# Performance work log

Hardware: AMD Instinct MI355X
Metric: run time of the kernel (lower is better)

Reference implementation:

```python
import jax, jax.numpy as jnp
import numpy as np

S, E, H, T = 8192, 100, 768, 7  # seq_len, embed_dim, per-dir hidden, tagset


def setup_inputs() -> dict:
    key = jax.random.key(0)
    ks = jax.random.split(key, 16)
    s = 0.05
    return {
        "sentence": jax.random.normal(ks[0], (S, 1, E), dtype=jnp.float32),
        # forward-direction LSTM params (PyTorch gate order i,f,g,o)
        "w_ih_f": jax.random.normal(ks[1], (4 * H, E), dtype=jnp.float32) * s,
        "w_hh_f": jax.random.normal(ks[2], (4 * H, H), dtype=jnp.float32) * s,
        "b_ih_f": jnp.zeros((4 * H,), jnp.float32),
        "b_hh_f": jnp.zeros((4 * H,), jnp.float32),
        # backward-direction LSTM params
        "w_ih_b": jax.random.normal(ks[3], (4 * H, E), dtype=jnp.float32) * s,
        "w_hh_b": jax.random.normal(ks[4], (4 * H, H), dtype=jnp.float32) * s,
        "b_ih_b": jnp.zeros((4 * H,), jnp.float32),
        "b_hh_b": jnp.zeros((4 * H,), jnp.float32),
        # random initial states, as in init_hidden() (shape (2,1,H): dir, batch, H)
        "h0": jax.random.normal(ks[5], (2, 1, H), dtype=jnp.float32),
        "c0": jax.random.normal(ks[6], (2, 1, H), dtype=jnp.float32),
        # hidden2tag linear
        "w_tag": jax.random.normal(ks[7], (T, 2 * H), dtype=jnp.float32) * s,
        "b_tag": jnp.zeros((T,), jnp.float32),
        # CRF params
        "transitions": jax.random.normal(ks[8], (T, T), dtype=jnp.float32) * 0.1,
        "start_trans": jax.random.normal(ks[9], (T,), dtype=jnp.float32) * 0.1,
        "end_trans": jax.random.normal(ks[10], (T,), dtype=jnp.float32) * 0.1,
    }


def _lstm_dir(x, w_ih, w_hh, b_ih, b_hh, h0, c0):
    """Single-direction LSTM. x: (S,E); returns hidden states (S,H)."""
    xp = x @ w_ih.T + b_ih  # (S, 4H) input projection, one big GEMM

    def step(carry, xt):
        h, c = carry
        g = xt + h @ w_hh.T + b_hh
        i, f, gg, o = jnp.split(g, 4)
        i = jax.nn.sigmoid(i)
        f = jax.nn.sigmoid(f)
        gg = jnp.tanh(gg)
        o = jax.nn.sigmoid(o)
        c = f * c + i * gg
        h = o * jnp.tanh(c)
        return (h, c), h

    _, hs = jax.lax.scan(step, (h0, c0), xp)
    return hs


def reference(sentence, w_ih_f, w_hh_f, b_ih_f, b_hh_f,
              w_ih_b, w_hh_b, b_ih_b, b_hh_b, h0, c0,
              w_tag, b_tag, transitions, start_trans, end_trans):
    x = sentence[:, 0, :]  # (S, E), batch of 1
    hf = _lstm_dir(x, w_ih_f, w_hh_f, b_ih_f, b_hh_f, h0[0, 0], c0[0, 0])
    hb = _lstm_dir(x[::-1], w_ih_b, w_hh_b, b_ih_b, b_hh_b, h0[1, 0], c0[1, 0])[::-1]
    lstm_out = jnp.concatenate([hf, hb], axis=-1)  # (S, 2H)
    feats = lstm_out @ w_tag.T + b_tag             # (S, T) emission scores

    # CRF forward algorithm (log-partition) -- sequential DP over tiny tagset
    alpha0 = start_trans + feats[0]

    def crf_step(alpha, emit):
        alpha = jax.nn.logsumexp(alpha[:, None] + transitions + emit[None, :], axis=0)
        return alpha, None

    alpha, _ = jax.lax.scan(crf_step, alpha0, feats[1:])
    return jax.nn.logsumexp(alpha + end_trans)  # scalar log Z
```

## Files before the change

kernel.cpp:

```cpp
#include <hip/hip_runtime.h>
#include <stdint.h>

#define S_LEN 8192
#define E_DIM 100
#define H_DIM 768
#define NTAG 7
#define G4 3072
#define NBLK 96
#define NCHUNK 128
#define POLL_LIMIT 150000

typedef unsigned short u16;
typedef unsigned long long u64;
typedef __attribute__((ext_vector_type(4))) float f4v;

__device__ int g_isbf16;

__device__ __forceinline__ u16 f2bf(float f) {
    union { float f; unsigned u; } v; v.f = f;
    unsigned b = v.u;
    unsigned r = (b + 0x7FFFu + ((b >> 16) & 1u)) >> 16;
    return (u16)r;
}
__device__ __forceinline__ float bf2f(u16 u) {
    union { unsigned u; float f; } v; v.u = ((unsigned)u) << 16;
    return v.f;
}
__device__ __forceinline__ float getv(const void* p, size_t i, int isbf) {
    return isbf ? bf2f(((const u16*)p)[i]) : ((const float*)p)[i];
}
__device__ __forceinline__ float sigm(float x) {
    return __builtin_amdgcn_rcpf(1.0f + __expf(-x));
}
__device__ __forceinline__ float ftanh(float x) {
    return 2.0f * __builtin_amdgcn_rcpf(1.0f + __expf(-2.0f * x)) - 1.0f;
}

__global__ void detect(const void* x) {
    __shared__ int cnt;
    if (threadIdx.x == 0) cnt = 0;
    __syncthreads();
    unsigned v = ((const u16*)x)[2 * threadIdx.x];
    int e = (v >> 7) & 0xFF;
    if (e >= 110 && e <= 132) atomicAdd(&cnt, 1);
    __syncthreads();
    if (threadIdx.x == 0) g_isbf16 = (cnt >= 100) ? 1 : 0;
}

__global__ void prep(const void* bihf, const void* bhhf,
                     const void* bihb, const void* bhhb,
                     const void* h0, const void* c0,
                     float* __restrict__ cst, float* __restrict__ bias,
                     u64* __restrict__ slots) {
    const int isbf = g_isbf16;
    int i = blockIdx.x * blockDim.x + threadIdx.x;
    if (i < G4) {
        bias[i]      = getv(bihf, i, isbf) + getv(bhhf, i, isbf);
        bias[G4 + i] = getv(bihb, i, isbf) + getv(bhhb, i, isbf);
    }
    if (i < 2 * H_DIM) cst[i] = getv(c0, i, isbf);
    if (i < 384) {
        unsigned pf = (unsigned)f2bf(getv(h0, 2 * i, isbf))
                    | ((unsigned)f2bf(getv(h0, 2 * i + 1, isbf)) << 16);
        unsigned pb = (unsigned)f2bf(getv(h0, H_DIM + 2 * i, isbf))
                    | ((unsigned)f2bf(getv(h0, H_DIM + 2 * i + 1, isbf)) << 16);
        slots[i]        = (u64)pf;
        slots[768 + i]  = (u64)pb;
        slots[384 + i]  = 0xFFFFFFFF00000000ull;
        slots[1152 + i] = 0xFFFFFFFF00000000ull;
    }
}

#define PISSUE(A, B)                                                     \
    asm volatile("global_load_dwordx2 %0, %2, off sc0 sc1\n\t"           \
                 "global_load_dwordx2 %1, %3, off sc0 sc1"               \
                 : "=&v"(A), "=&v"(B) : "v"(pa), "v"(pb) : "memory")
#define PWAIT2(A, B)                                                     \
    asm volatile("s_waitcnt vmcnt(2)" : "+v"(A), "+v"(B))
#define PDRAIN4(A, B, C, D)                                              \
    asm volatile("s_waitcnt vmcnt(0)"                                    \
                 : "+v"(A), "+v"(B), "+v"(C), "+v"(D))

__global__ __launch_bounds__(256, 1) void lstm_persist(
        const void* x,
        const void* wihf, const void* whhf,
        const void* wihb, const void* whhb,
        u16* __restrict__ hfseq, u16* __restrict__ hbseq,
        float* __restrict__ cstate, const float* __restrict__ biasv,
        u64* __restrict__ slots, int* __restrict__ bail) {
    const int isbf = g_isbf16;
    const int bid = blockIdx.x;
    const int dir = (bid >= NBLK) ? 1 : 0;
    const int blk = bid - dir * NBLK;
    const int tid = threadIdx.x;
    const int wave = tid >> 6, lane = tid & 63;
    const int seg = tid & 7;
    const int row = tid >> 3;
    const int gamma = row & 3;
    const int uloc = row >> 2;
    const int u = blk * 8 + uloc;
    const size_t grow = (size_t)(gamma * H_DIM + u);
    u16* hseq = dir ? hbseq : hfseq;
    u64* myslots = slots + (size_t)dir * 768;
    const void* Wih = dir ? wihb : wihf;
    const void* Whh = dir ? whhb : whhf;

    __shared__ float sh[1600];

    float whh[96], wih[13];
    if (isbf) {
        const unsigned* p = (const unsigned*)((const u16*)Whh + grow * H_DIM + seg * 96);
        #pragma unroll
        for (int i = 0; i < 48; ++i) {
            unsigned q = p[i];
            whh[2 * i] = bf2f((u16)q); whh[2 * i + 1] = bf2f((u16)(q >> 16));
        }
        const unsigned* px = (const unsigned*)((const u16*)Wih + grow * E_DIM + seg * 12);
        #pragma unroll
        for (int i = 0; i < 6; ++i) {
            unsigned q = px[i];
            wih[2 * i] = bf2f((u16)q); wih[2 * i + 1] = bf2f((u16)(q >> 16));
        }
        wih[12] = (seg < 4) ? bf2f(((const u16*)Wih)[grow * E_DIM + 96 + seg]) : 0.f;
    } else {
        const float* p = (const float*)Whh + grow * H_DIM + seg * 96;
        #pragma unroll
        for (int i = 0; i < 96; ++i) whh[i] = p[i];
        const float* px = (const float*)Wih + grow * E_DIM + seg * 12;
        #pragma unroll
        for (int i = 0; i < 12; ++i) wih[i] = px[i];
        wih[12] = (seg < 4) ? ((const float*)Wih)[grow * E_DIM + 96 + seg] : 0.f;
    }
    const float bias_r = biasv[dir * G4 + grow];
    const int uhalf = blk * 8 + wave * 2 + (lane >> 5);
    float cst = cstate[dir * H_DIM + uhalf];

    const int sA = wave * 96 + lane;
    const int sB = (lane < 32) ? (wave * 96 + 64 + lane) : sA;
    const int oA = (2 * wave + (lane >= 48)) * 100 + 2 * lane - ((lane >= 48) ? 96 : 0);
    const int oB = (2 * wave + 1) * 100 + 32 + 2 * lane;
    const int pubslot = blk * 4 + wave;

    float    xf[13];
    unsigned xu[6];
    u16      xt16 = 0;
    auto load_x = [&](int t) {
        const int sx = dir ? (S_LEN - 1 - t) : t;
        if (isbf) {
            const unsigned* xr = (const unsigned*)((const u16*)x + (size_t)sx * E_DIM + seg * 12);
            #pragma unroll
            for (int i = 0; i < 6; ++i) xu[i] = xr[i];
            if (seg < 4) xt16 = ((const u16*)x)[(size_t)sx * E_DIM + 96 + seg];
        } else {
            const float* xr = (const float*)x + (size_t)sx * E_DIM + seg * 12;
            #pragma unroll
            for (int i = 0; i < 12; ++i) xf[i] = xr[i];
            xf[12] = (seg < 4) ? ((const float*)x)[(size_t)sx * E_DIM + 96 + seg] : 0.f;
        }
    };
    auto fma_x = [&]() -> float {
        float ax = 0.f;
        if (isbf) {
            #pragma unroll
            for (int i = 0; i < 6; ++i) {
                unsigned q = xu[i];
                ax += wih[2 * i] * bf2f((u16)q) + wih[2 * i + 1] * bf2f((u16)(q >> 16));
            }
            if (seg < 4) ax += wih[12] * bf2f(xt16);
        } else {
            #pragma unroll
            for (int i = 0; i < 12; ++i) ax += wih[i] * xf[i];
            ax += wih[12] * xf[12];
        }
        return ax;
    };

    load_x(0);

    for (int t = 0; t < S_LEN; ++t) {
        float ax = fma_x();

        u64 va = 0, vb = 0;
        {
            const u64* buf = myslots + (size_t)(t & 1) * 384;
            const u64* pa = buf + sA;
            const u64* pb = buf + sB;
            const unsigned tgt = (unsigned)t;
            u64 a0, b0, a1, b1;
            int polls = 0;
            bool found = false;
            asm volatile("s_waitcnt vmcnt(0)" ::: "memory");
            for (;;) {
                PISSUE(a0, b0);
                for (int it = 0; it < 32; ++it) {
                    PISSUE(a1, b1);
                    PWAIT2(a0, b0);
                    if (__all(((unsigned)(a0 >> 32) == tgt) &
                              ((unsigned)(b0 >> 32) == tgt))) {
                        va = a0; vb = b0; found = true; break;
                    }
                    PISSUE(a0, b0);
                    PWAIT2(a1, b1);
                    if (__all(((unsigned)(a1 >> 32) == tgt) &
                              ((unsigned)(b1 >> 32) == tgt))) {
                        va = a1; vb = b1; found = true; break;
                    }
                }
                PDRAIN4(a0, b0, a1, b1);
                if (found) break;
                u64 f0 = __hip_atomic_load(&buf[sA], __ATOMIC_RELAXED,
                                           __HIP_MEMORY_SCOPE_AGENT);
                u64 f1 = __hip_atomic_load(&buf[sB], __ATOMIC_RELAXED,
                                           __HIP_MEMORY_SCOPE_AGENT);
                if (__all(((unsigned)(f0 >> 32) == tgt) &
                          ((unsigned)(f1 >> 32) == tgt))) {
                    va = f0; vb = f1; break;
                }
                polls += 64;
                if (__hip_atomic_load(bail, __ATOMIC_RELAXED,
                                      __HIP_MEMORY_SCOPE_AGENT)) {
                    va = f0; vb = f1; break;
                }
                if (polls > POLL_LIMIT) {
                    __hip_atomic_store(bail, 1, __ATOMIC_RELAXED,
                                       __HIP_MEMORY_SCOPE_AGENT);
                    va = f0; vb = f1; break;
                }
                __builtin_amdgcn_s_sleep(2);
            }

            float* shb = sh + (t & 1) * 800;
            unsigned p0 = (unsigned)va;
            shb[oA]     = bf2f((u16)p0);
            shb[oA + 1] = bf2f((u16)(p0 >> 16));
            if (lane < 32) {
                unsigned p1 = (unsigned)vb;
                shb[oB]     = bf2f((u16)p1);
                shb[oB + 1] = bf2f((u16)(p1 >> 16));
            }
        }
        __syncthreads();

        load_x((t + 1 < S_LEN) ? (t + 1) : t);

        const float* hs = sh + (t & 1) * 800 + seg * 100;
        float a0 = 0.f, a1 = 0.f, a2 = 0.f, a3 = 0.f;
        #pragma unroll
        for (int i = 0; i < 24; ++i) {
            f4v hv = *(const f4v*)(hs + 4 * i);
            a0 += whh[4 * i]     * hv.x;
            a1 += whh[4 * i + 1] * hv.y;
            a2 += whh[4 * i + 2] * hv.z;
            a3 += whh[4 * i + 3] * hv.w;
        }
        float acc = ax + (a0 + a1) + (a2 + a3);
        acc += __shfl_xor(acc, 1);
        acc += __shfl_xor(acc, 2);
        acc += __shfl_xor(acc, 4);
        float g = acc + bias_r;

        const int base = lane & 32;
        float gi = __shfl(g, base + 0);
        float gf = __shfl(g, base + 8);
        float gg = __shfl(g, base + 16);
        float go = __shfl(g, base + 24);
        float ii = sigm(gi), ff = sigm(gf), gt = ftanh(gg), oo = sigm(go);
        float c = ff * cst + ii * gt;
        cst = c;
        float h = oo * ftanh(c);

        {
            float hodd = __shfl(h, 32);
            if (lane == 0) {
                unsigned pk = (unsigned)f2bf(h) | ((unsigned)f2bf(hodd) << 16);
                u64 sv = (((u64)(unsigned)(t + 1)) << 32) | (u64)pk;
                __hip_atomic_store(&myslots[(size_t)((t + 1) & 1) * 384 + pubslot],
                                   sv, __ATOMIC_RELAXED, __HIP_MEMORY_SCOPE_AGENT);
                __hip_atomic_store(
                    &((unsigned*)(hseq + (size_t)(t + 1) * H_DIM))[pubslot],
                    pk, __ATOMIC_RELAXED, __HIP_MEMORY_SCOPE_AGENT);
            }
        }
    }
}

__global__ __launch_bounds__(256) void feats_kernel(const u16* __restrict__ hfseq,
                                                    const u16* __restrict__ hbseq,
                                                    const void* w_tag, const void* b_tag,
                                                    float* __restrict__ feats) {
    const int isbf = g_isbf16;
    const int wave = threadIdx.x >> 6, lane = threadIdx.x & 63;
    const int s = blockIdx.x * 4 + wave;
    if (s >= S_LEN) return;
    const u16* hf = hfseq + (size_t)(s + 1) * H_DIM;
    const u16* hb = hbseq + (size_t)(S_LEN - s) * H_DIM;
    float hv[12], hbv[12];
    #pragma unroll
    for (int i = 0; i < 12; ++i) {
        hv[i]  = bf2f(hf[lane + 64 * i]);
        hbv[i] = bf2f(hb[lane + 64 * i]);
    }
    float myf = 0.f;
    for (int j = 0; j < NTAG; ++j) {
        const size_t wr = (size_t)j * (2 * H_DIM);
        float d = 0.f;
        #pragma unroll
        for (int i = 0; i < 12; ++i)
            d += hv[i] * getv(w_tag, wr + lane + 64 * i, isbf)
               + hbv[i] * getv(w_tag, wr + H_DIM + lane + 64 * i, isbf);
        #pragma unroll
        for (int m = 1; m < 64; m <<= 1) d += __shfl_xor(d, m);
        if (lane == j) myf = d + getv(b_tag, j, isbf);
    }
    if (lane < NTAG) feats[(size_t)s * NTAG + lane] = myf;
}

__global__ void crf_chunks(const void* trans,
                           const float* __restrict__ feats,
                           float* __restrict__ cmats) {
    const int isbf = g_isbf16;
    const int c = blockIdx.x;
    const int lane = threadIdx.x;
    const bool act = lane < 49;
    const int i = act ? (lane / 7) : 0;
    const int j = lane % 7;
    float tc[7];
    #pragma unroll
    for (int k = 0; k < 7; ++k) tc[k] = getv(trans, k * 7 + j, isbf);
    float R = (act && (lane / 7) == j) ? 0.f : -1e30f;
    int s0 = 1 + c * 64;
    int s1 = s0 + 64; if (s1 > S_LEN) s1 = S_LEN;
    for (int t = s0; t < s1; ++t) {
        float fj = feats[t * NTAG + j];
        float r[7];
        #pragma unroll
        for (int k = 0; k < 7; ++k) r[k] = __shfl(R, i * 7 + k) + tc[k];
        float m = r[0];
        #pragma unroll
        for (int k = 1; k < 7; ++k) m = fmaxf(m, r[k]);
        float sum = 0.f;
        #pragma unroll
        for (int k = 0; k < 7; ++k) sum += __expf(r[k] - m);
        R = m + __logf(sum) + fj;
    }
    if (act) cmats[c * 49 + lane] = R;
}

__global__ void crf_final(const void* start_t, const void* end_t,
                          const float* __restrict__ feats,
                          const float* __restrict__ cmats,
                          void* __restrict__ out) {
    const int isbf = g_isbf16;
    const int lane = threadIdx.x;
    const int j = (lane < 7) ? lane : 0;
    float alpha = (lane < 7) ? (getv(start_t, lane, isbf) + feats[lane]) : -1e30f;
    for (int c = 0; c < NCHUNK; ++c) {
        float r[7];
        #pragma unroll
        for (int i = 0; i < 7; ++i)
            r[i] = __shfl(alpha, i) + cmats[c * 49 + i * 7 + j];
        float m = r[0];
        #pragma unroll
        for (int i = 1; i < 7; ++i) m = fmaxf(m, r[i]);
        float sum = 0.f;
        #pragma unroll
        for (int i = 0; i < 7; ++i) sum += __expf(r[i] - m);
        float na = m + __logf(sum);
        alpha = (lane < 7) ? na : -1e30f;
    }
    float v = (lane < 7) ? (alpha + getv(end_t, lane, isbf)) : -1e30f;
    float m = v;
    #pragma unroll
    for (int d = 1; d < 8; d <<= 1) m = fmaxf(m, __shfl_xor(m, d));
    float s = __expf(v - m);
    #pragma unroll
    for (int d = 1; d < 8; d <<= 1) s += __shfl_xor(s, d);
    if (lane == 0) {
        float r = m + __logf(s);
        if (isbf) ((u16*)out)[0] = f2bf(r);
        else      ((float*)out)[0] = r;
    }
}

extern "C" void kernel_launch(void* const* d_in, const int* in_sizes, int n_in,
                              void* d_out, int out_size, void* d_ws, size_t ws_size,
                              hipStream_t stream) {
    const void* sentence = d_in[0];
    const void* w_ih_f   = d_in[1];
    const void* w_hh_f   = d_in[2];
    const void* b_ih_f   = d_in[3];
    const void* b_hh_f   = d_in[4];
    const void* w_ih_b   = d_in[5];
    const void* w_hh_b   = d_in[6];
    const void* b_ih_b   = d_in[7];
    const void* b_hh_b   = d_in[8];
    const void* h0       = d_in[9];
    const void* c0       = d_in[10];
    const void* w_tag    = d_in[11];
    const void* b_tag    = d_in[12];
    const void* trans    = d_in[13];
    const void* start_t  = d_in[14];
    const void* end_t    = d_in[15];
    (void)in_sizes; (void)n_in; (void)out_size; (void)ws_size;

    char* ws = (char*)d_ws;
    size_t o = 0;
    auto take = [&](size_t bytes) -> char* {
        char* p = ws + o;
        o += (bytes + 255) & ~(size_t)255;
        return p;
    };
    u16*   hfseq  = (u16*)take((size_t)(S_LEN + 1) * H_DIM * 2);
    u16*   hbseq  = (u16*)take((size_t)(S_LEN + 1) * H_DIM * 2);
    float* cstate = (float*)take((size_t)2 * H_DIM * 4);
    float* biasv  = (float*)take((size_t)2 * G4 * 4);
    float* featsb = (float*)take((size_t)S_LEN * NTAG * 4);
    float* cmats  = (float*)take((size_t)NCHUNK * 49 * 4);
    u64*   slots  = (u64*)take((size_t)2 * 2 * 384 * 8);
    int*   bail   = (int*)take((size_t)256 * 4);

    detect<<<1, 128, 0, stream>>>(sentence);
    prep<<<12, 256, 0, stream>>>(b_ih_f, b_hh_f, b_ih_b, b_hh_b, h0, c0,
                                 cstate, biasv, slots);
    (void)hipMemsetAsync(bail, 0, 4, stream);

    lstm_persist<<<2 * NBLK, 256, 0, stream>>>(sentence,
                                               w_ih_f, w_hh_f, w_ih_b, w_hh_b,
                                               hfseq, hbseq, cstate, biasv,
                                               slots, bail);

    feats_kernel<<<S_LEN / 4, 256, 0, stream>>>(hfseq, hbseq, w_tag, b_tag, featsb);
    crf_chunks<<<NCHUNK, 64, 0, stream>>>(trans, featsb, cmats);
    crf_final<<<1, 64, 0, stream>>>(start_t, end_t, featsb, cmats, d_out);
}
```

Before: 15.86 ms.

## Remap LSTM threads so each half-wave owns one unit's four gates

Reassigns work in the persistent LSTM kernel so that each 32-lane half-wave computes all four gates of one hidden unit. Each lane holds a 24-element slice of the hidden vector and reads it once from shared memory as float2, reusing it across the four gates. This replaces the old 8-lane segment split, which needed a 3-step reduction and then four cross-lane shuffles to gather the gates. The shared buffer is padded (26-float stride) to avoid bank conflicts. The cost is a deeper 5-step butterfly reduction over four accumulators (20 shuffles) and an input projection where only 25 of 32 lanes are active.

```diff
diff --git a/kernel.cpp b/kernel.cpp
--- a/kernel.cpp
+++ b/kernel.cpp
@@ -13,6 +13,7 @@
 typedef unsigned short u16;
 typedef unsigned long long u64;
 typedef __attribute__((ext_vector_type(4))) float f4v;
+typedef __attribute__((ext_vector_type(2))) float f2v;
 
 __device__ int g_isbf16;
 
@@ -94,91 +95,108 @@
     const int blk = bid - dir * NBLK;
     const int tid = threadIdx.x;
     const int wave = tid >> 6, lane = tid & 63;
-    const int seg = tid & 7;
-    const int row = tid >> 3;
-    const int gamma = row & 3;
-    const int uloc = row >> 2;
+    const int half = (tid >> 5) & 1;
+    const int jj = tid & 31;
+    const int uloc = wave * 2 + half;
     const int u = blk * 8 + uloc;
-    const size_t grow = (size_t)(gamma * H_DIM + u);
     u16* hseq = dir ? hbseq : hfseq;
     u64* myslots = slots + (size_t)dir * 768;
     const void* Wih = dir ? wihb : wihf;
     const void* Whh = dir ? whhb : whhf;
 
-    __shared__ float sh[1600];
-
-    float whh[96], wih[13];
+    __shared__ float sh[2 * 832];
+
+    float whh[96], wih[16];
+    #pragma unroll
+    for (int i = 0; i < 16; ++i) wih[i] = 0.f;
     if (isbf) {
-        const unsigned* p = (const unsigned*)((const u16*)Whh + grow * H_DIM + seg * 96);
-        #pragma unroll
-        for (int i = 0; i < 48; ++i) {
-            unsigned q = p[i];
-            whh[2 * i] = bf2f((u16)q); whh[2 * i + 1] = bf2f((u16)(q >> 16));
-        }
-        const unsigned* px = (const unsigned*)((const u16*)Wih + grow * E_DIM + seg * 12);
-        #pragma unroll
-        for (int i = 0; i < 6; ++i) {
-            unsigned q = px[i];
-            wih[2 * i] = bf2f((u16)q); wih[2 * i + 1] = bf2f((u16)(q >> 16));
-        }
-        wih[12] = (seg < 4) ? bf2f(((const u16*)Wih)[grow * E_DIM + 96 + seg]) : 0.f;
+        #pragma unroll
+        for (int g = 0; g < 4; ++g) {
+            const unsigned* p = (const unsigned*)((const u16*)Whh
+                              + (size_t)(g * H_DIM + u) * H_DIM + jj * 24);
+            #pragma unroll
+            for (int i = 0; i < 12; ++i) {
+                unsigned q = p[i];
+                whh[g * 24 + 2 * i]     = bf2f((u16)q);
+                whh[g * 24 + 2 * i + 1] = bf2f((u16)(q >> 16));
+            }
+        }
+        if (jj < 25) {
+            #pragma unroll
+            for (int g = 0; g < 4; ++g) {
+                const unsigned* q = (const unsigned*)((const u16*)Wih
+                                  + (size_t)(g * H_DIM + u) * E_DIM + 4 * jj);
+                unsigned q0 = q[0], q1 = q[1];
+                wih[g * 4 + 0] = bf2f((u16)q0);
+                wih[g * 4 + 1] = bf2f((u16)(q0 >> 16));
+                wih[g * 4 + 2] = bf2f((u16)q1);
+                wih[g * 4 + 3] = bf2f((u16)(q1 >> 16));
+            }
+        }
     } else {
-        const float* p = (const float*)Whh + grow * H_DIM + seg * 96;
-        #pragma unroll
-        for (int i = 0; i < 96; ++i) whh[i] = p[i];
-        const float* px = (const float*)Wih + grow * E_DIM + seg * 12;
-        #pragma unroll
-        for (int i = 0; i < 12; ++i) wih[i] = px[i];
-        wih[12] = (seg < 4) ? ((const float*)Wih)[grow * E_DIM + 96 + seg] : 0.f;
-    }
-    const float bias_r = biasv[dir * G4 + grow];
-    const int uhalf = blk * 8 + wave * 2 + (lane >> 5);
-    float cst = cstate[dir * H_DIM + uhalf];
+        #pragma unroll
+        for (int g = 0; g < 4; ++g) {
+            const float* p = (const float*)Whh
+                           + (size_t)(g * H_DIM + u) * H_DIM + jj * 24;
+            #pragma unroll
+            for (int i = 0; i < 24; ++i) whh[g * 24 + i] = p[i];
+        }
+        if (jj < 25) {
+            #pragma unroll
+            for (int g = 0; g < 4; ++g) {
+                const float* q = (const float*)Wih
+                               + (size_t)(g * H_DIM + u) * E_DIM + 4 * jj;
+                wih[g * 4 + 0] = q[0]; wih[g * 4 + 1] = q[1];
+                wih[g * 4 + 2] = q[2]; wih[g * 4 + 3] = q[3];
+            }
+        }
+    }
+    float b0r = biasv[dir * G4 + 0 * H_DIM + u];
+    float b1r = biasv[dir * G4 + 1 * H_DIM + u];
+    float b2r = biasv[dir * G4 + 2 * H_DIM + u];
+    float b3r = biasv[dir * G4 + 3 * H_DIM + u];
+    float cst = cstate[dir * H_DIM + u];
 
     const int sA = wave * 96 + lane;
     const int sB = (lane < 32) ? (wave * 96 + 64 + lane) : sA;
-    const int oA = (2 * wave + (lane >= 48)) * 100 + 2 * lane - ((lane >= 48) ? 96 : 0);
-    const int oB = (2 * wave + 1) * 100 + 32 + 2 * lane;
+    const int kA = 2 * sA, kB = 2 * sB;
+    const int oA = (kA / 24) * 26 + kA % 24;
+    const int oB = (kB / 24) * 26 + kB % 24;
     const int pubslot = blk * 4 + wave;
 
-    float    xf[13];
-    unsigned xu[6];
-    u16      xt16 = 0;
+    float    xf[4];
+    unsigned xu[2];
     auto load_x = [&](int t) {
         const int sx = dir ? (S_LEN - 1 - t) : t;
-        if (isbf) {
-            const unsigned* xr = (const unsigned*)((const u16*)x + (size_t)sx * E_DIM + seg * 12);
-            #pragma unroll
-            for (int i = 0; i < 6; ++i) xu[i] = xr[i];
-            if (seg < 4) xt16 = ((const u16*)x)[(size_t)sx * E_DIM + 96 + seg];
-        } else {
-            const float* xr = (const float*)x + (size_t)sx * E_DIM + seg * 12;
-            #pragma unroll
-            for (int i = 0; i < 12; ++i) xf[i] = xr[i];
-            xf[12] = (seg < 4) ? ((const float*)x)[(size_t)sx * E_DIM + 96 + seg] : 0.f;
+        if (jj < 25) {
+            if (isbf) {
+                const unsigned* p = (const unsigned*)((const u16*)x
+                                  + (size_t)sx * E_DIM + 4 * jj);
+                xu[0] = p[0]; xu[1] = p[1];
+            } else {
+                f4v v = *(const f4v*)((const float*)x + (size_t)sx * E_DIM + 4 * jj);
+                xf[0] = v.x; xf[1] = v.y; xf[2] = v.z; xf[3] = v.w;
+            }
         }
     };
-    auto fma_x = [&]() -> float {
-        float ax = 0.f;
-        if (isbf) {
-            #pragma unroll
-            for (int i = 0; i < 6; ++i) {
-                unsigned q = xu[i];
-                ax += wih[2 * i] * bf2f((u16)q) + wih[2 * i + 1] * bf2f((u16)(q >> 16));
-            }
-            if (seg < 4) ax += wih[12] * bf2f(xt16);
-        } else {
-            #pragma unroll
-            for (int i = 0; i < 12; ++i) ax += wih[i] * xf[i];
-            ax += wih[12] * xf[12];
-        }
-        return ax;
-    };
 
     load_x(0);
 
     for (int t = 0; t < S_LEN; ++t) {
-        float ax = fma_x();
+        float a0 = 0.f, a1 = 0.f, a2 = 0.f, a3 = 0.f;
+        if (jj < 25) {
+            float x0, x1, x2, x3;
+            if (isbf) {
+                x0 = bf2f((u16)xu[0]); x1 = bf2f((u16)(xu[0] >> 16));
+                x2 = bf2f((u16)xu[1]); x3 = bf2f((u16)(xu[1] >> 16));
+            } else {
+                x0 = xf[0]; x1 = xf[1]; x2 = xf[2]; x3 = xf[3];
+            }
+            a0 = wih[0]  * x0 + wih[1]  * x1 + wih[2]  * x2 + wih[3]  * x3;
+            a1 = wih[4]  * x0 + wih[5]  * x1 + wih[6]  * x2 + wih[7]  * x3;
+            a2 = wih[8]  * x0 + wih[9]  * x1 + wih[10] * x2 + wih[11] * x3;
+            a3 = wih[12] * x0 + wih[13] * x1 + wih[14] * x2 + wih[15] * x3;
+        }
 
         u64 va = 0, vb = 0;
         {
@@ -186,27 +204,27 @@
             const u64* pa = buf + sA;
             const u64* pb = buf + sB;
             const unsigned tgt = (unsigned)t;
-            u64 a0, b0, a1, b1;
+            u64 a0p, b0p, a1p, b1p;
             int polls = 0;
             bool found = false;
             asm volatile("s_waitcnt vmcnt(0)" ::: "memory");
             for (;;) {
-                PISSUE(a0, b0);
+                PISSUE(a0p, b0p);
                 for (int it = 0; it < 32; ++it) {
-                    PISSUE(a1, b1);
-                    PWAIT2(a0, b0);
-                    if (__all(((unsigned)(a0 >> 32) == tgt) &
-                              ((unsigned)(b0 >> 32) == tgt))) {
-                        va = a0; vb = b0; found = true; break;
+                    PISSUE(a1p, b1p);
+                    PWAIT2(a0p, b0p);
+                    if (__all(((unsigned)(a0p >> 32) == tgt) &
+                              ((unsigned)(b0p >> 32) == tgt))) {
+                        va = a0p; vb = b0p; found = true; break;
                     }
-                    PISSUE(a0, b0);
-                    PWAIT2(a1, b1);
-                    if (__all(((unsigned)(a1 >> 32) == tgt) &
-                              ((unsigned)(b1 >> 32) == tgt))) {
-                        va = a1; vb = b1; found = true; break;
+                    PISSUE(a0p, b0p);
+                    PWAIT2(a1p, b1p);
+                    if (__all(((unsigned)(a1p >> 32) == tgt) &
+                              ((unsigned)(b1p >> 32) == tgt))) {
+                        va = a1p; vb = b1p; found = true; break;
                     }
                 }
-                PDRAIN4(a0, b0, a1, b1);
+                PDRAIN4(a0p, b0p, a1p, b1p);
                 if (found) break;
                 u64 f0 = __hip_atomic_load(&buf[sA], __ATOMIC_RELAXED,
                                            __HIP_MEMORY_SCOPE_AGENT);
@@ -229,7 +247,7 @@
                 __builtin_amdgcn_s_sleep(2);
             }
 
-            float* shb = sh + (t & 1) * 800;
+            float* shb = sh + (t & 1) * 832;
             unsigned p0 = (unsigned)va;
             shb[oA]     = bf2f((u16)p0);
             shb[oA + 1] = bf2f((u16)(p0 >> 16));
@@ -243,28 +261,26 @@
 
         load_x((t + 1 < S_LEN) ? (t + 1) : t);
 
-        const float* hs = sh + (t & 1) * 800 + seg * 100;
-        float a0 = 0.f, a1 = 0.f, a2 = 0.f, a3 = 0.f;
-        #pragma unroll
-        for (int i = 0; i < 24; ++i) {
-            f4v hv = *(const f4v*)(hs + 4 * i);
-            a0 += whh[4 * i]     * hv.x;
-            a1 += whh[4 * i + 1] * hv.y;
-            a2 += whh[4 * i + 2] * hv.z;
-            a3 += whh[4 * i + 3] * hv.w;
-        }
-        float acc = ax + (a0 + a1) + (a2 + a3);
-        acc += __shfl_xor(acc, 1);
-        acc += __shfl_xor(acc, 2);
-        acc += __shfl_xor(acc, 4);
-        float g = acc + bias_r;
-
-        const int base = lane & 32;
-        float gi = __shfl(g, base + 0);
-        float gf = __shfl(g, base + 8);
-        float gg = __shfl(g, base + 16);
-        float go = __shfl(g, base + 24);
-        float ii = sigm(gi), ff = sigm(gf), gt = ftanh(gg), oo = sigm(go);
+        const f2v* h2 = (const f2v*)(sh + (t & 1) * 832 + jj * 26);
+        #pragma unroll
+        for (int i = 0; i < 12; ++i) {
+            f2v hv = h2[i];
+            a0 += whh[2 * i]      * hv.x + whh[2 * i + 1]      * hv.y;
+            a1 += whh[24 + 2 * i] * hv.x + whh[24 + 2 * i + 1] * hv.y;
+            a2 += whh[48 + 2 * i] * hv.x + whh[48 + 2 * i + 1] * hv.y;
+            a3 += whh[72 + 2 * i] * hv.x + whh[72 + 2 * i + 1] * hv.y;
+        }
+
+        #pragma unroll
+        for (int m = 1; m <= 16; m <<= 1) {
+            a0 += __shfl_xor(a0, m);
+            a1 += __shfl_xor(a1, m);
+            a2 += __shfl_xor(a2, m);
+            a3 += __shfl_xor(a3, m);
+        }
+
+        float ii = sigm(a0 + b0r), ff = sigm(a1 + b1r);
+        float gt = ftanh(a2 + b2r), oo = sigm(a3 + b3r);
         float c = ff * cst + ii * gt;
         cst = c;
         float h = oo * ftanh(c);
```

After: 17.37 ms. 9.5% more time.

## Replicate hidden-state publish slots four ways to spread polling contention

Applied to the files above, without the earlier changes.

Each block now polls one of four replicated copies of the step-synchronisation slot buffer, picked by block index. The producer writes each published hidden-state value to all four replicas. The aim is to cut contention from 192 blocks polling the same cache lines every timestep. In exchange, every publish costs four stores, and the replicas may not be visible at the same time. The oA/oB offset formulas are rewritten in an equivalent general form.

```diff
diff --git a/kernel.cpp b/kernel.cpp
--- a/kernel.cpp
+++ b/kernel.cpp
@@ -9,6 +9,8 @@
 #define NBLK 96
 #define NCHUNK 128
 #define POLL_LIMIT 150000
+#define NREP 4
+#define REPSTRIDE 1536
 
 typedef unsigned short u16;
 typedef unsigned long long u64;
@@ -64,10 +66,14 @@
                     | ((unsigned)f2bf(getv(h0, 2 * i + 1, isbf)) << 16);
         unsigned pb = (unsigned)f2bf(getv(h0, H_DIM + 2 * i, isbf))
                     | ((unsigned)f2bf(getv(h0, H_DIM + 2 * i + 1, isbf)) << 16);
-        slots[i]        = (u64)pf;
-        slots[768 + i]  = (u64)pb;
-        slots[384 + i]  = 0xFFFFFFFF00000000ull;
-        slots[1152 + i] = 0xFFFFFFFF00000000ull;
+        #pragma unroll
+        for (int r = 0; r < NREP; ++r) {
+            u64* rb = slots + (size_t)r * REPSTRIDE;
+            rb[i]        = (u64)pf;
+            rb[768 + i]  = (u64)pb;
+            rb[384 + i]  = 0xFFFFFFFF00000000ull;
+            rb[1152 + i] = 0xFFFFFFFF00000000ull;
+        }
     }
 }
 
@@ -101,7 +107,8 @@
     const int u = blk * 8 + uloc;
     const size_t grow = (size_t)(gamma * H_DIM + u);
     u16* hseq = dir ? hbseq : hfseq;
-    u64* myslots = slots + (size_t)dir * 768;
+    u64* myslots = slots + (size_t)(blk & 3) * REPSTRIDE + (size_t)dir * 768;
+    u64* pubbase = slots + (size_t)dir * 768;
     const void* Wih = dir ? wihb : wihf;
     const void* Whh = dir ? whhb : whhf;
 
@@ -137,8 +144,9 @@
 
     const int sA = wave * 96 + lane;
     const int sB = (lane < 32) ? (wave * 96 + 64 + lane) : sA;
-    const int oA = (2 * wave + (lane >= 48)) * 100 + 2 * lane - ((lane >= 48) ? 96 : 0);
-    const int oB = (2 * wave + 1) * 100 + 32 + 2 * lane;
+    const int kA = 2 * sA, kB = 2 * sB;
+    const int oA = (kA / 96) * 100 + kA % 96;
+    const int oB = (kB / 96) * 100 + kB % 96;
     const int pubslot = blk * 4 + wave;
 
     float    xf[13];
@@ -186,27 +194,27 @@
             const u64* pa = buf + sA;
             const u64* pb = buf + sB;
             const unsigned tgt = (unsigned)t;
-            u64 a0, b0, a1, b1;
+            u64 a0p, b0p, a1p, b1p;
             int polls = 0;
             bool found = false;
             asm volatile("s_waitcnt vmcnt(0)" ::: "memory");
             for (;;) {
-                PISSUE(a0, b0);
+                PISSUE(a0p, b0p);
                 for (int it = 0; it < 32; ++it) {
-                    PISSUE(a1, b1);
-                    PWAIT2(a0, b0);
-                    if (__all(((unsigned)(a0 >> 32) == tgt) &
-                              ((unsigned)(b0 >> 32) == tgt))) {
-                        va = a0; vb = b0; found = true; break;
+                    PISSUE(a1p, b1p);
+                    PWAIT2(a0p, b0p);
+                    if (__all(((unsigned)(a0p >> 32) == tgt) &
+                              ((unsigned)(b0p >> 32) == tgt))) {
+                        va = a0p; vb = b0p; found = true; break;
                     }
-                    PISSUE(a0, b0);
-                    PWAIT2(a1, b1);
-                    if (__all(((unsigned)(a1 >> 32) == tgt) &
-                              ((unsigned)(b1 >> 32) == tgt))) {
-                        va = a1; vb = b1; found = true; break;
+                    PISSUE(a0p, b0p);
+                    PWAIT2(a1p, b1p);
+                    if (__all(((unsigned)(a1p >> 32) == tgt) &
+                              ((unsigned)(b1p >> 32) == tgt))) {
+                        va = a1p; vb = b1p; found = true; break;
                     }
                 }
-                PDRAIN4(a0, b0, a1, b1);
+                PDRAIN4(a0p, b0p, a1p, b1p);
                 if (found) break;
                 u64 f0 = __hip_atomic_load(&buf[sA], __ATOMIC_RELAXED,
                                            __HIP_MEMORY_SCOPE_AGENT);
@@ -274,8 +282,11 @@
             if (lane == 0) {
                 unsigned pk = (unsigned)f2bf(h) | ((unsigned)f2bf(hodd) << 16);
                 u64 sv = (((u64)(unsigned)(t + 1)) << 32) | (u64)pk;
-                __hip_atomic_store(&myslots[(size_t)((t + 1) & 1) * 384 + pubslot],
-                                   sv, __ATOMIC_RELAXED, __HIP_MEMORY_SCOPE_AGENT);
+                u64* dst = pubbase + (size_t)((t + 1) & 1) * 384 + pubslot;
+                #pragma unroll
+                for (int r = 0; r < NREP; ++r)
+                    __hip_atomic_store(dst + (size_t)r * REPSTRIDE, sv,
+                                       __ATOMIC_RELAXED, __HIP_MEMORY_SCOPE_AGENT);
                 __hip_atomic_store(
                     &((unsigned*)(hseq + (size_t)(t + 1) * H_DIM))[pubslot],
                     pk, __ATOMIC_RELAXED, __HIP_MEMORY_SCOPE_AGENT);
@@ -416,7 +427,7 @@
     float* biasv  = (float*)take((size_t)2 * G4 * 4);
     float* featsb = (float*)take((size_t)S_LEN * NTAG * 4);
     float* cmats  = (float*)take((size_t)NCHUNK * 49 * 4);
-    u64*   slots  = (u64*)take((size_t)2 * 2 * 384 * 8);
+    u64*   slots  = (u64*)take((size_t)NREP * REPSTRIDE * 8);
     int*   bail   = (int*)take((size_t)256 * 4);
 
     detect<<<1, 128, 0, stream>>>(sentence);
```

Result: faster. 15.18 ms (-4.3%).
